# Kernel tuning notes

Hardware: AMD Instinct MI355X
Metric: run time of the kernel (lower is better)

Reference implementation:

```python
import jax, jax.numpy as jnp
import numpy as np

SAMPLE_RATE = 44100
HOP_LENGTH = 256
N_HARMONICS = 64


def _linear_interp_last(x, out_len):
    """F.interpolate(mode='bilinear', align_corners=True) with the height axis
    kept at its original size reduces to 1-D linear interpolation (align_corners)
    along the last axis."""
    t = x.shape[-1]
    pos = jnp.arange(out_len, dtype=x.dtype) * ((t - 1) / (out_len - 1))
    i0 = jnp.clip(jnp.floor(pos).astype(jnp.int32), 0, t - 2)
    w = pos - i0.astype(x.dtype)
    return x[..., i0] * (1.0 - w) + x[..., i0 + 1] * w


def setup_inputs() -> dict:
    key = jax.random.key(0)
    k1, k2, k3, k4 = jax.random.split(key, 4)
    b, c, o, t = 4, 1, N_HARMONICS, 1025
    # f0 in a realistic 50..450 Hz range so the Nyquist mask is exercised
    f0 = jax.random.uniform(k1, (b, c, t), dtype=jnp.float32) * 400.0 + 50.0
    master_amplitude = jax.random.uniform(k2, (b, c, t), dtype=jnp.float32)
    overtone_amplitudes = jax.random.uniform(k3, (b, c, o, t), dtype=jnp.float32)
    # uniform [0,1) used for the random initial phase pi*(2u-1)
    init_phase_u = jax.random.uniform(k4, (b, c, o), dtype=jnp.float32)
    return {
        "f0": f0,
        "master_amplitude": master_amplitude,
        "overtone_amplitudes": overtone_amplitudes,
        "init_phase_u": init_phase_u,
    }


def reference(f0, master_amplitude, overtone_amplitudes, init_phase_u):
    b, c, t = f0.shape
    harmonics = jnp.arange(1, N_HARMONICS + 1, dtype=f0.dtype)  # [o]
    # angular frequency per sample: [b,c,o,t]
    fs = jnp.einsum('bct,o->bcot', f0, harmonics) * (2.0 * np.pi / SAMPLE_RATE)
    # zero out harmonics above Nyquist, then normalize over harmonics
    amps = jnp.where(fs > np.pi, 0.0, overtone_amplitudes)
    amps = amps / jnp.sum(amps, axis=2, keepdims=True)
    amps = amps * master_amplitude[:, :, None, :]
    # upsample frame-rate -> sample-rate along time (align_corners bilinear)
    out_len = (t - 1) * HOP_LENGTH
    fs_up = _linear_interp_last(fs, out_len)      # [b,c,o,T]
    amps_up = _linear_interp_last(amps, out_len)  # [b,c,o,T]
    # random initial phase in (-pi, pi) at sample 0, then phase accumulation
    fs_up = fs_up.at[..., 0].set(3.14159265 * (init_phase_u * 2.0 - 1.0))
    phases = jnp.cumsum(fs_up, axis=-1)
    # sin, amplitude-weight, sum over harmonics: [b,c,T]
    signal = jnp.sum(jnp.sin(phases) * amps_up, axis=2)
    return signal
```

## Files before the change

kernel.cpp:

```cpp
#include <hip/hip_runtime.h>
#include <math.h>
#include <stdint.h>

#define B    4
#define O    64
#define TF   1025
#define NF   1024
#define NF2  2048
#define NQ   4096
#define TOUT 262144

#define C32POS  ((float)(1024.0 / 262143.0))
#define C2PI32  ((float)(2.0 * M_PI / 44100.0))
#define PI32    ((float)M_PI)
#define INV2PI32 ((float)(1.0 / (2.0 * M_PI)))
#define INV2PI64 0.15915494309189535

__device__ __forceinline__ float lin32(float x0, float x1, float w) {
    float omw = 1.0f - w;
    float t1 = x0 * omw;
    float t2 = x1 * w;
    asm volatile("" : "+v"(t1), "+v"(t2));
    return t1 + t2;
}

__device__ __forceinline__ float init32(float uu) {
    return ((uu * 2.0f) - 1.0f) * PI32;
}

__device__ __forceinline__ float fract32(float x) {
#if __has_builtin(__builtin_amdgcn_fractf)
    return __builtin_amdgcn_fractf(x);
#else
    return x - floorf(x);
#endif
}

__global__ void __launch_bounds__(64) k1(
        const float* __restrict__ f0, const float* __restrict__ master,
        const float* __restrict__ ov,
        float* __restrict__ FS, float* __restrict__ Aamp) {
    int f = blockIdx.x, b = blockIdx.y, o = threadIdx.x;
    float f0v = f0[b * TF + f];
    float fs  = (f0v * (float)(o + 1)) * C2PI32;
    FS[(b * O + o) * TF + f] = fs;
    float val = (fs > PI32) ? 0.0f : ov[(b * O + o) * TF + f];
    float den = val;
    #pragma unroll
    for (int d = 32; d; d >>= 1) den += __shfl_xor(den, d, 64);
    Aamp[(b * O + o) * TF + f] = (val / den) * master[b * TF + f];
}

__global__ void __launch_bounds__(256) kT(const float* __restrict__ FS,
                                          const float* __restrict__ u,
                                          double* __restrict__ T) {
    int f = blockIdx.x, b = blockIdx.y;
    int t = threadIdx.x;
    int o = t & 63, q = t >> 6;
    int chain = b * O + o;
    float fs0 = FS[chain * TF + f], fs1 = FS[chain * TF + f + 1];
    float ff = (float)f;
    float fn = (float)(f * 256 + q * 64);
    double s = 0.0;
    #pragma unroll 8
    for (int k = 0; k < 64; ++k) {
        float pos = fn * C32POS;
        asm volatile("" : "+v"(pos));
        float w = pos - ff;
        s += (double)lin32(fs0, fs1, w);
        fn += 1.0f;
    }
    if (f == 0 && q == 0)
        s = s - (double)fs0 + (double)init32(u[chain]);
    T[(size_t)chain * NQ + f * 4 + q] = s;
}

__global__ void __launch_bounds__(256) kScan(const double* __restrict__ T,
                                             double* __restrict__ C) {
    int chain = blockIdx.x, t = threadIdx.x;
    const double* Tc = T + (size_t)chain * NQ;
    double v[16], tot = 0.0;
    #pragma unroll
    for (int m = 0; m < 16; ++m) { v[m] = Tc[t * 16 + m]; tot += v[m]; }
    __shared__ double sb[256];
    sb[t] = tot;
    __syncthreads();
    for (int off = 1; off < 256; off <<= 1) {
        double x = (t >= off) ? sb[t - off] : 0.0;
        __syncthreads();
        sb[t] += x;
        __syncthreads();
    }
    double run = sb[t] - tot;
    double* Cc = C + (size_t)chain * NQ;
    #pragma unroll
    for (int m = 0; m < 16; ++m) { Cc[t * 16 + m] = run; run += v[m]; }
}

__global__ void __launch_bounds__(256, 8) kC(const float* __restrict__ FS,
                                             const float* __restrict__ Aamp,
                                             const float* __restrict__ u,
                                             const double* __restrict__ C,
                                             float* __restrict__ out) {
    __shared__ float scal[4][O][8];
    int t = threadIdx.x;
    int lane = t & 63, wv = t >> 6;
    int task = blockIdx.x * 4 + wv;
    int fh = task & (NF2 - 1);
    int b  = task >> 11;
    int f  = fh >> 1;
    int chain_l = b * O + lane;

    const float* FSc = FS + chain_l * TF;
    const float* Ac  = Aamp + chain_l * TF;
    float fs0 = FSc[f], fs1 = FSc[f + 1];
    float a0  = Ac[f],  a1  = Ac[f + 1];
    const double* Cc = C + (size_t)chain_l * NQ + fh * 2;
    double c0 = Cc[0] * INV2PI64;
    double c1 = Cc[1] * INV2PI64;
    float vC0 = (float)(c0 - rint(c0));
    float vC1 = (float)(c1 - rint(c1));
    float vF  = fs0 * INV2PI32;
    float vD  = (fs1 - fs0) * INV2PI32;
    if (fh == 0)
        vC0 = vC0 + (init32(u[chain_l]) - fs0) * INV2PI32;
    *(float4*)&scal[wv][lane][0] = make_float4(vC0, vC1, vF, vD);
    *(float2*)&scal[wv][lane][4] = make_float2(a0, a1 - a0);

    int n0 = fh * 128 + lane;
    float ff = (float)f;
    float pos0 = (float)n0 * C32POS;
    asm volatile("" : "+v"(pos0));
    float w0 = pos0 - ff;
    float pos1 = (float)(n0 + 64) * C32POS;
    asm volatile("" : "+v"(pos1));
    float w1 = pos1 - ff;

    float W0 = w0, W1 = w1;
    #pragma unroll
    for (int d = 1; d < 64; d <<= 1) {
        float s0 = __shfl_up(W0, d, 64);
        float s1 = __shfl_up(W1, d, 64);
        if (lane >= d) { W0 += s0; W1 += s1; }
    }
    float cntf = (float)(lane + 1);
    __syncthreads();

    float acc0 = 0.0f, acc1 = 0.0f;
    #pragma unroll 8
    for (int o = 0; o < O; ++o) {
        float4 s4 = *(const float4*)&scal[wv][o][0];
        float2 s2 = *(const float2*)&scal[wv][o][4];
        float u0  = fmaf(W0, s4.w, s4.x);
        float ph0 = fmaf(cntf, s4.z, u0);
        float am0 = fmaf(w0, s2.y, s2.x);
        acc0 = fmaf(__builtin_amdgcn_sinf(fract32(ph0)), am0, acc0);
        float u1  = fmaf(W1, s4.w, s4.y);
        float ph1 = fmaf(cntf, s4.z, u1);
        float am1 = fmaf(w1, s2.y, s2.x);
        acc1 = fmaf(__builtin_amdgcn_sinf(fract32(ph1)), am1, acc1);
    }
    size_t ob = (size_t)b * TOUT + fh * 128;
    out[ob + lane]      = acc0;
    out[ob + 64 + lane] = acc1;
}

extern "C" void kernel_launch(void* const* d_in, const int* in_sizes, int n_in,
                              void* d_out, int out_size, void* d_ws, size_t ws_size,
                              hipStream_t stream) {
    const float* f0     = (const float*)d_in[0];
    const float* master = (const float*)d_in[1];
    const float* ov     = (const float*)d_in[2];
    const float* u      = (const float*)d_in[3];
    float* out = (float*)d_out;

    double* T    = (double*)d_ws;
    double* C    = T + (size_t)B * O * NQ;
    float*  FS   = (float*)(C + (size_t)B * O * NQ);
    float*  Aamp = FS + (size_t)B * O * TF;

    k1   <<<dim3(TF, B),      64,  0, stream>>>(f0, master, ov, FS, Aamp);
    kT   <<<dim3(NF, B),      256, 0, stream>>>(FS, u, T);
    kScan<<<B * O,            256, 0, stream>>>(T, C);
    kC   <<<(B * NF2) / 4,    256, 0, stream>>>(FS, Aamp, u, C, out);
}
```

Baseline: 52.04 us.

## Recompute harmonic frequencies from f0 and store amplitudes frame-major for coalescing

Drops the FS intermediate buffer entirely; kT and kC recompute per-harmonic angular frequency from f0 instead of loading it, removing one global write and several strided reads. The amplitude buffer changes to a [frame][batch][harmonic] layout so writes in k1 and reads in kC are coalesced across lanes. kT precomputes interpolation weights once into shared memory, which adds a block barrier. kC's occupancy hint drops from 8 to 4 and its unroll from 8 to 4, which changes register pressure and scheduling.

```diff
diff --git a/kernel.cpp b/kernel.cpp
--- a/kernel.cpp
+++ b/kernel.cpp
@@ -38,38 +38,39 @@
 
 __global__ void __launch_bounds__(64) k1(
         const float* __restrict__ f0, const float* __restrict__ master,
-        const float* __restrict__ ov,
-        float* __restrict__ FS, float* __restrict__ Aamp) {
+        const float* __restrict__ ov, float* __restrict__ Aamp) {
     int f = blockIdx.x, b = blockIdx.y, o = threadIdx.x;
     float f0v = f0[b * TF + f];
     float fs  = (f0v * (float)(o + 1)) * C2PI32;
-    FS[(b * O + o) * TF + f] = fs;
     float val = (fs > PI32) ? 0.0f : ov[(b * O + o) * TF + f];
     float den = val;
     #pragma unroll
     for (int d = 32; d; d >>= 1) den += __shfl_xor(den, d, 64);
-    Aamp[(b * O + o) * TF + f] = (val / den) * master[b * TF + f];
+    Aamp[(f * B + b) * O + o] = (val / den) * master[b * TF + f];
 }
 
-__global__ void __launch_bounds__(256) kT(const float* __restrict__ FS,
+__global__ void __launch_bounds__(256) kT(const float* __restrict__ f0,
                                           const float* __restrict__ u,
                                           double* __restrict__ T) {
+    __shared__ float wlds[4][64];
     int f = blockIdx.x, b = blockIdx.y;
     int t = threadIdx.x;
     int o = t & 63, q = t >> 6;
+    {
+        float pos = (float)(f * 256 + q * 64 + o) * C32POS;
+        asm volatile("" : "+v"(pos));
+        wlds[q][o] = pos - (float)f;
+    }
+    __syncthreads();
     int chain = b * O + o;
-    float fs0 = FS[chain * TF + f], fs1 = FS[chain * TF + f + 1];
-    float ff = (float)f;
-    float fn = (float)(f * 256 + q * 64);
+    float f00 = f0[b * TF + f], f01 = f0[b * TF + f + 1];
+    float hm  = (float)(o + 1);
+    float fs0 = (f00 * hm) * C2PI32;
+    float fs1 = (f01 * hm) * C2PI32;
     double s = 0.0;
     #pragma unroll 8
-    for (int k = 0; k < 64; ++k) {
-        float pos = fn * C32POS;
-        asm volatile("" : "+v"(pos));
-        float w = pos - ff;
-        s += (double)lin32(fs0, fs1, w);
-        fn += 1.0f;
-    }
+    for (int k = 0; k < 64; ++k)
+        s += (double)lin32(fs0, fs1, wlds[q][k]);
     if (f == 0 && q == 0)
         s = s - (double)fs0 + (double)init32(u[chain]);
     T[(size_t)chain * NQ + f * 4 + q] = s;
@@ -97,7 +98,7 @@
     for (int m = 0; m < 16; ++m) { Cc[t * 16 + m] = run; run += v[m]; }
 }
 
-__global__ void __launch_bounds__(256, 8) kC(const float* __restrict__ FS,
+__global__ void __launch_bounds__(256, 4) kC(const float* __restrict__ f0,
                                              const float* __restrict__ Aamp,
                                              const float* __restrict__ u,
                                              const double* __restrict__ C,
@@ -111,10 +112,12 @@
     int f  = fh >> 1;
     int chain_l = b * O + lane;
 
-    const float* FSc = FS + chain_l * TF;
-    const float* Ac  = Aamp + chain_l * TF;
-    float fs0 = FSc[f], fs1 = FSc[f + 1];
-    float a0  = Ac[f],  a1  = Ac[f + 1];
+    float f00 = f0[b * TF + f], f01 = f0[b * TF + f + 1];
+    float hm  = (float)(lane + 1);
+    float fs0 = (f00 * hm) * C2PI32;
+    float fs1 = (f01 * hm) * C2PI32;
+    float a0  = Aamp[(f * B + b) * O + lane];
+    float a1  = Aamp[((f + 1) * B + b) * O + lane];
     const double* Cc = C + (size_t)chain_l * NQ + fh * 2;
     double c0 = Cc[0] * INV2PI64;
     double c1 = Cc[1] * INV2PI64;
@@ -147,7 +150,7 @@
     __syncthreads();
 
     float acc0 = 0.0f, acc1 = 0.0f;
-    #pragma unroll 8
+    #pragma unroll 4
     for (int o = 0; o < O; ++o) {
         float4 s4 = *(const float4*)&scal[wv][o][0];
         float2 s2 = *(const float2*)&scal[wv][o][4];
@@ -176,11 +179,10 @@
 
     double* T    = (double*)d_ws;
     double* C    = T + (size_t)B * O * NQ;
-    float*  FS   = (float*)(C + (size_t)B * O * NQ);
-    float*  Aamp = FS + (size_t)B * O * TF;
+    float*  Aamp = (float*)(C + (size_t)B * O * NQ);
 
-    k1   <<<dim3(TF, B),      64,  0, stream>>>(f0, master, ov, FS, Aamp);
-    kT   <<<dim3(NF, B),      256, 0, stream>>>(FS, u, T);
+    k1   <<<dim3(TF, B),      64,  0, stream>>>(f0, master, ov, Aamp);
+    kT   <<<dim3(NF, B),      256, 0, stream>>>(f0, u, T);
     kScan<<<B * O,            256, 0, stream>>>(T, C);
-    kC   <<<(B * NF2) / 4,    256, 0, stream>>>(FS, Aamp, u, C, out);
+    kC   <<<(B * NF2) / 4,    256, 0, stream>>>(f0, Aamp, u, C, out);
 }
```

After: 47.71 us. -8.3%, faster.
